# Performance work log

Measured on AMD Instinct MI355X. Metric: run time of the kernel, lower is better.

Reference implementation:

```python
import jax, jax.numpy as jnp
import numpy as np

N_NODES = 100000
F_IN = 64
F_OUT = 64
SLOPE = 0.2


def setup_inputs() -> dict:
    key = jax.random.key(0)
    k1, k2, k3, k4 = jax.random.split(key, 4)
    input_matrix = jax.random.normal(k1, (N_NODES, F_IN), dtype=jnp.float32)
    edge_index = jax.random.randint(k2, (2, 1600000), 0, N_NODES, dtype=jnp.int64)
    # xavier-uniform-style params
    lim_w = float(np.sqrt(6.0 / (F_IN + F_OUT)))
    W = jax.random.uniform(k3, (F_IN, F_OUT), minval=-lim_w, maxval=lim_w, dtype=jnp.float32)
    lim_a = float(np.sqrt(6.0 / (2 * F_OUT + 1)))
    a = jax.random.uniform(k4, (2 * F_OUT,), minval=-lim_a, maxval=lim_a, dtype=jnp.float32)
    return {"input_matrix": input_matrix, "edge_index": edge_index, "W": W, "a": a}


def reference(input_matrix, edge_index, W, a):
    N = input_matrix.shape[0]
    # add self edges
    loops = jnp.arange(N, dtype=edge_index.dtype)
    src = jnp.concatenate([edge_index[0], loops])  # [E+N]
    dst = jnp.concatenate([edge_index[1], loops])  # [E+N]

    h = input_matrix @ W                      # [N, F_out]
    F = h.shape[1]
    h_src = h[src]                            # [E+N, F_out] gather
    h_dst = h[dst]                            # [E+N, F_out] gather
    # cat([h_src, h_dst], 1) @ a == h_src @ a[:F] + h_dst @ a[F:]
    alpha = h_src @ a[:F] + h_dst @ a[F:]     # [E+N]
    alpha = jnp.where(alpha >= 0, alpha, SLOPE * alpha)  # leaky relu
    alpha = jnp.exp(alpha)
    denom = jax.ops.segment_sum(alpha, src, num_segments=N)  # [N]
    alpha = alpha / denom[src]                # segment softmax over edges sharing src
    out = jax.ops.segment_sum(h_dst * alpha[:, None], src, num_segments=N)  # [N, F_out]
    return out
```

## Files before the change

### kernel.cpp

```cpp
#include <hip/hip_runtime.h>
#include <hip/hip_bf16.h>

#define F 64
#define SLOPE 0.2f
#define NB_SHIFT 8
#define BATCH 4096
#define HIST_BLOCKS 128

typedef __attribute__((ext_vector_type(8))) short bf16x8;
typedef __attribute__((ext_vector_type(4))) float f32x4;

__device__ inline unsigned short f2bf(float f) {
    unsigned u = __float_as_uint(f);
    unsigned r = (u + 0x7FFFu + ((u >> 16) & 1u)) >> 16;
    return (unsigned short)r;
}

__global__ __launch_bounds__(256) void gat_histb(
    const int* __restrict__ src, int* __restrict__ partialHist, int E,
    const float* __restrict__ W, const float* __restrict__ a,
    unsigned short* __restrict__ Wp, float* __restrict__ w1,
    float* __restrict__ w2) {
    __shared__ int lh[512];
    int tid = threadIdx.x;
    for (int i = tid; i < 512; i += 256) lh[i] = 0;
    __syncthreads();
    for (int i = blockIdx.x * 256 + tid; i < E; i += HIST_BLOCKS * 256)
        atomicAdd(&lh[src[i] >> NB_SHIFT], 1);
    __syncthreads();
    for (int i = tid; i < 512; i += 256)
        partialHist[blockIdx.x * 512 + i] = lh[i];

    if (blockIdx.x == 0) {
        if (tid < 64) {
#pragma unroll
            for (int f = 0; f < 8; ++f) {
                int cg = f >> 1, kc = f & 1;
                int col = cg * 16 + (tid & 15);
                unsigned short us[8];
#pragma unroll
                for (int j = 0; j < 8; ++j) {
                    int k = kc * 32 + (tid >> 4) * 8 + j;
                    us[j] = f2bf(W[k * F + col]);
                }
                uint4 pk;
                pk.x = us[0] | ((unsigned)us[1] << 16);
                pk.y = us[2] | ((unsigned)us[3] << 16);
                pk.z = us[4] | ((unsigned)us[5] << 16);
                pk.w = us[6] | ((unsigned)us[7] << 16);
                *(uint4*)&Wp[(f * 64 + tid) * 8] = pk;
            }
        } else if (tid < 128) {
            int k = tid - 64;
            float acc1 = 0.f, acc2 = 0.f;
#pragma unroll
            for (int n = 0; n < F; ++n) {
                float wv = W[k * F + n];
                acc1 = fmaf(wv, a[n], acc1);
                acc2 = fmaf(wv, a[F + n], acc2);
            }
            w1[k] = acc1;
            w2[k] = acc2;
        }
    }
}

__global__ __launch_bounds__(256) void gat_gemm_mfma(
    const float* __restrict__ X, const unsigned short* __restrict__ Wp,
    const float* __restrict__ w1, const float* __restrict__ w2,
    unsigned short* __restrict__ hb, float* __restrict__ s1,
    float* __restrict__ s2, int N) {
    int tid = threadIdx.x;
    int lane = tid & 63;
    int wv = tid >> 6;
    int rowBase = blockIdx.x * 64 + wv * 16;
    if (rowBase >= N) return;
    int lrow = lane & 15;
    int kg = lane >> 4;
    int row = rowBase + lrow;
    int rclamp = (row < N) ? row : (N - 1);

    const float* xp = &X[(size_t)rclamp * F + kg * 8];
    float4 u0 = *(const float4*)(xp + 0);
    float4 u1 = *(const float4*)(xp + 4);
    float4 u2 = *(const float4*)(xp + 32);
    float4 u3 = *(const float4*)(xp + 36);
    float xr[16] = {u0.x, u0.y, u0.z, u0.w, u1.x, u1.y, u1.z, u1.w,
                    u2.x, u2.y, u2.z, u2.w, u3.x, u3.y, u3.z, u3.w};

    bf16x8 a0, a1;
#pragma unroll
    for (int j = 0; j < 8; ++j) {
        a0[j] = (short)f2bf(xr[j]);
        a1[j] = (short)f2bf(xr[8 + j]);
    }

    bf16x8 bf0 = *(const bf16x8*)&Wp[(0 * 64 + lane) * 8];
    bf16x8 bf1 = *(const bf16x8*)&Wp[(1 * 64 + lane) * 8];
    bf16x8 bf2 = *(const bf16x8*)&Wp[(2 * 64 + lane) * 8];
    bf16x8 bf3 = *(const bf16x8*)&Wp[(3 * 64 + lane) * 8];
    bf16x8 bf4 = *(const bf16x8*)&Wp[(4 * 64 + lane) * 8];
    bf16x8 bf5 = *(const bf16x8*)&Wp[(5 * 64 + lane) * 8];
    bf16x8 bf6 = *(const bf16x8*)&Wp[(6 * 64 + lane) * 8];
    bf16x8 bf7 = *(const bf16x8*)&Wp[(7 * 64 + lane) * 8];

    f32x4 acc0 = {0.f, 0.f, 0.f, 0.f};
    f32x4 acc1v = {0.f, 0.f, 0.f, 0.f};
    f32x4 acc2v = {0.f, 0.f, 0.f, 0.f};
    f32x4 acc3 = {0.f, 0.f, 0.f, 0.f};
    acc0 = __builtin_amdgcn_mfma_f32_16x16x32_bf16(a0, bf0, acc0, 0, 0, 0);
    acc0 = __builtin_amdgcn_mfma_f32_16x16x32_bf16(a1, bf1, acc0, 0, 0, 0);
    acc1v = __builtin_amdgcn_mfma_f32_16x16x32_bf16(a0, bf2, acc1v, 0, 0, 0);
    acc1v = __builtin_amdgcn_mfma_f32_16x16x32_bf16(a1, bf3, acc1v, 0, 0, 0);
    acc2v = __builtin_amdgcn_mfma_f32_16x16x32_bf16(a0, bf4, acc2v, 0, 0, 0);
    acc2v = __builtin_amdgcn_mfma_f32_16x16x32_bf16(a1, bf5, acc2v, 0, 0, 0);
    acc3 = __builtin_amdgcn_mfma_f32_16x16x32_bf16(a0, bf6, acc3, 0, 0, 0);
    acc3 = __builtin_amdgcn_mfma_f32_16x16x32_bf16(a1, bf7, acc3, 0, 0, 0);

#pragma unroll
    for (int r = 0; r < 4; ++r) {
        int ro = rowBase + kg * 4 + r;
        if (ro < N) {
            size_t rb = (size_t)ro * F + lrow;
            hb[rb + 0] = f2bf(acc0[r]);
            hb[rb + 16] = f2bf(acc1v[r]);
            hb[rb + 32] = f2bf(acc2v[r]);
            hb[rb + 48] = f2bf(acc3[r]);
        }
    }

    float4 wa0 = *(const float4*)&w1[kg * 8];
    float4 wa1 = *(const float4*)&w1[kg * 8 + 4];
    float4 wa2 = *(const float4*)&w1[32 + kg * 8];
    float4 wa3 = *(const float4*)&w1[32 + kg * 8 + 4];
    float4 wb0 = *(const float4*)&w2[kg * 8];
    float4 wb1 = *(const float4*)&w2[kg * 8 + 4];
    float4 wb2 = *(const float4*)&w2[32 + kg * 8];
    float4 wb3 = *(const float4*)&w2[32 + kg * 8 + 4];
    float wv1[16] = {wa0.x, wa0.y, wa0.z, wa0.w, wa1.x, wa1.y, wa1.z, wa1.w,
                     wa2.x, wa2.y, wa2.z, wa2.w, wa3.x, wa3.y, wa3.z, wa3.w};
    float wv2[16] = {wb0.x, wb0.y, wb0.z, wb0.w, wb1.x, wb1.y, wb1.z, wb1.w,
                     wb2.x, wb2.y, wb2.z, wb2.w, wb3.x, wb3.y, wb3.z, wb3.w};
    float p = 0.f, q = 0.f;
#pragma unroll
    for (int j = 0; j < 16; ++j) {
        p = fmaf(xr[j], wv1[j], p);
        q = fmaf(xr[j], wv2[j], q);
    }
    p += __shfl_xor(p, 16, 64);
    p += __shfl_xor(p, 32, 64);
    q += __shfl_xor(q, 16, 64);
    q += __shfl_xor(q, 32, 64);
    if (lane < 16 && row < N) {
        s1[row] = p;
        s2[row] = q;
    }
}

__global__ __launch_bounds__(512) void gat_scan0(
    const int* __restrict__ partialHist, int* __restrict__ bucketBase,
    int* __restrict__ bucketCursor, int* __restrict__ rowptrN, int NB) {
    __shared__ int wsum[8];
    int tid = threadIdx.x, lane = tid & 63, wid = tid >> 6;
    int v = 0;
    for (int p = 0; p < HIST_BLOCKS; ++p)
        v += partialHist[p * 512 + tid];
    int x = v;
#pragma unroll
    for (int off = 1; off < 64; off <<= 1) {
        int y = __shfl_up(x, off, 64);
        if (lane >= off) x += y;
    }
    if (lane == 63) wsum[wid] = x;
    __syncthreads();
    int add = 0;
    for (int w = 0; w < 8; ++w)
        if (w < wid) add += wsum[w];
    int excl = add + x - v;
    if (tid < NB) {
        bucketBase[tid] = excl;
        bucketCursor[tid] = excl;
    }
    if (tid == NB - 1) {
        bucketBase[NB] = excl + v;
        rowptrN[0] = excl + v;
    }
}

__global__ __launch_bounds__(512) void gat_bin(
    const int* __restrict__ src, const int* __restrict__ dst,
    int* __restrict__ bucketCursor, unsigned* __restrict__ bucketData, int E) {
    __shared__ int hist[512], excl[512], gbase[512], cur[512];
    __shared__ int wsum[8];
    __shared__ int2 staged[BATCH];
    int tid = threadIdx.x, lane = tid & 63, wid = tid >> 6;
    int base = blockIdx.x * BATCH;
    int n = E - base;
    if (n > BATCH) n = BATCH;

    hist[tid] = 0;
    __syncthreads();

    int se[8], de[8];
#pragma unroll
    for (int j = 0; j < 8; ++j) {
        int i = base + j * 512 + tid;
        se[j] = -1;
        de[j] = 0;
        if (i < E) {
            se[j] = src[i];
            de[j] = dst[i];
            atomicAdd(&hist[se[j] >> NB_SHIFT], 1);
        }
    }
    __syncthreads();
    int v = hist[tid];
    int x = v;
#pragma unroll
    for (int off = 1; off < 64; off <<= 1) {
        int y = __shfl_up(x, off, 64);
        if (lane >= off) x += y;
    }
    if (lane == 63) wsum[wid] = x;
    __syncthreads();
    int add = 0;
    for (int w = 0; w < 8; ++w)
        if (w < wid) add += wsum[w];
    int ex = add + x - v;
    excl[tid] = ex;
    cur[tid] = ex;
    __syncthreads();
#pragma unroll
    for (int j = 0; j < 8; ++j) {
        if (se[j] >= 0) {
            int b = se[j] >> NB_SHIFT;
            int pos = atomicAdd(&cur[b], 1);
            staged[pos] = make_int2(se[j], de[j]);
        }
    }
    if (v > 0)
        gbase[tid] = atomicAdd(&bucketCursor[tid], v);
    __syncthreads();
    for (int i = tid; i < n; i += 512) {
        int2 p = staged[i];
        int b = p.x >> NB_SHIFT;
        bucketData[gbase[b] + (i - excl[b])] =
            ((unsigned)(p.x & 255) << 24) | (unsigned)p.y;
    }
}

__global__ __launch_bounds__(256) void gat_bucket(
    const int* __restrict__ bucketBase, const unsigned* __restrict__ bucketData,
    int* __restrict__ rowptr, int* __restrict__ sortedDst, int N) {
    __shared__ int cnt[256], cur[256];
    __shared__ int wsum[4];
    int b = blockIdx.x;
    int tid = threadIdx.x, lane = tid & 63, wid = tid >> 6;
    int beg = bucketBase[b];
    int end = bucketBase[b + 1];
    int node0 = b << NB_SHIFT;

    cnt[tid] = 0;
    __syncthreads();
    for (int i = beg + tid; i < end; i += 256)
        atomicAdd(&cnt[bucketData[i] >> 24], 1);
    __syncthreads();
    int v = cnt[tid];
    int x = v;
#pragma unroll
    for (int off = 1; off < 64; off <<= 1) {
        int y = __shfl_up(x, off, 64);
        if (lane >= off) x += y;
    }
    if (lane == 63) wsum[wid] = x;
    __syncthreads();
    int add = 0;
    for (int w = 0; w < 4; ++w)
        if (w < wid) add += wsum[w];
    int excl = add + x - v;
    int node = node0 + tid;
    if (node < N) rowptr[node] = beg + excl;
    cur[tid] = beg + excl;
    __syncthreads();
    for (int i = beg + tid; i < end; i += 256) {
        unsigned w = bucketData[i];
        int pos = atomicAdd(&cur[w >> 24], 1);
        sortedDst[pos] = (int)(w & 0xFFFFFFu);
    }
}

__global__ __launch_bounds__(256) void gat_aggregate(
    const int* __restrict__ rowptr,
    const int* __restrict__ sortedDst,
    const float* __restrict__ s1, const float* __restrict__ s2,
    const unsigned short* __restrict__ hb, float* __restrict__ out, int N) {
    int tid = threadIdx.x;
    int node = blockIdx.x * 32 + (tid >> 3);
    if (node >= N) return;
    const int fo = (tid & 7) * 8;

    int beg = rowptr[node];
    int end = rowptr[node + 1];
    float s1s = s1[node];
    float as = s1s + s2[node];
    as = (as >= 0.f) ? as : SLOPE * as;
    as = expf(as);

    float accA[8], accB[8];
    {
        uint4 hv = *(const uint4*)&hb[(size_t)node * F + fo];
        accA[0] = as * __uint_as_float(hv.x << 16);
        accA[1] = as * __uint_as_float(hv.x & 0xFFFF0000u);
        accA[2] = as * __uint_as_float(hv.y << 16);
        accA[3] = as * __uint_as_float(hv.y & 0xFFFF0000u);
        accA[4] = as * __uint_as_float(hv.z << 16);
        accA[5] = as * __uint_as_float(hv.z & 0xFFFF0000u);
        accA[6] = as * __uint_as_float(hv.w << 16);
        accA[7] = as * __uint_as_float(hv.w & 0xFFFF0000u);
    }
#pragma unroll
    for (int i = 0; i < 8; ++i) accB[i] = 0.f;

    float dsum = as;
    int e = beg;
    for (; e + 2 <= end; e += 2) {
        int d0 = sortedDst[e];
        int d1 = sortedDst[e + 1];
        float t0 = s1s + s2[d0];
        float t1 = s1s + s2[d1];
        t0 = (t0 >= 0.f) ? t0 : SLOPE * t0;
        t1 = (t1 >= 0.f) ? t1 : SLOPE * t1;
        float a0 = expf(t0);
        float a1 = expf(t1);
        dsum += a0 + a1;
        uint4 g0 = *(const uint4*)&hb[(size_t)d0 * F + fo];
        uint4 g1 = *(const uint4*)&hb[(size_t)d1 * F + fo];
        accA[0] = fmaf(a0, __uint_as_float(g0.x << 16), accA[0]);
        accA[1] = fmaf(a0, __uint_as_float(g0.x & 0xFFFF0000u), accA[1]);
        accA[2] = fmaf(a0, __uint_as_float(g0.y << 16), accA[2]);
        accA[3] = fmaf(a0, __uint_as_float(g0.y & 0xFFFF0000u), accA[3]);
        accA[4] = fmaf(a0, __uint_as_float(g0.z << 16), accA[4]);
        accA[5] = fmaf(a0, __uint_as_float(g0.z & 0xFFFF0000u), accA[5]);
        accA[6] = fmaf(a0, __uint_as_float(g0.w << 16), accA[6]);
        accA[7] = fmaf(a0, __uint_as_float(g0.w & 0xFFFF0000u), accA[7]);
        accB[0] = fmaf(a1, __uint_as_float(g1.x << 16), accB[0]);
        accB[1] = fmaf(a1, __uint_as_float(g1.x & 0xFFFF0000u), accB[1]);
        accB[2] = fmaf(a1, __uint_as_float(g1.y << 16), accB[2]);
        accB[3] = fmaf(a1, __uint_as_float(g1.y & 0xFFFF0000u), accB[3]);
        accB[4] = fmaf(a1, __uint_as_float(g1.z << 16), accB[4]);
        accB[5] = fmaf(a1, __uint_as_float(g1.z & 0xFFFF0000u), accB[5]);
        accB[6] = fmaf(a1, __uint_as_float(g1.w << 16), accB[6]);
        accB[7] = fmaf(a1, __uint_as_float(g1.w & 0xFFFF0000u), accB[7]);
    }
    if (e < end) {
        int d0 = sortedDst[e];
        float t0 = s1s + s2[d0];
        t0 = (t0 >= 0.f) ? t0 : SLOPE * t0;
        float a0 = expf(t0);
        dsum += a0;
        uint4 g0 = *(const uint4*)&hb[(size_t)d0 * F + fo];
        accA[0] = fmaf(a0, __uint_as_float(g0.x << 16), accA[0]);
        accA[1] = fmaf(a0, __uint_as_float(g0.x & 0xFFFF0000u), accA[1]);
        accA[2] = fmaf(a0, __uint_as_float(g0.y << 16), accA[2]);
        accA[3] = fmaf(a0, __uint_as_float(g0.y & 0xFFFF0000u), accA[3]);
        accA[4] = fmaf(a0, __uint_as_float(g0.z << 16), accA[4]);
        accA[5] = fmaf(a0, __uint_as_float(g0.z & 0xFFFF0000u), accA[5]);
        accA[6] = fmaf(a0, __uint_as_float(g0.w << 16), accA[6]);
        accA[7] = fmaf(a0, __uint_as_float(g0.w & 0xFFFF0000u), accA[7]);
    }

    float inv = 1.0f / dsum;
    float4 r0, r1;
    r0.x = (accA[0] + accB[0]) * inv;
    r0.y = (accA[1] + accB[1]) * inv;
    r0.z = (accA[2] + accB[2]) * inv;
    r0.w = (accA[3] + accB[3]) * inv;
    r1.x = (accA[4] + accB[4]) * inv;
    r1.y = (accA[5] + accB[5]) * inv;
    r1.z = (accA[6] + accB[6]) * inv;
    r1.w = (accA[7] + accB[7]) * inv;
    *(float4*)&out[(size_t)node * F + fo] = r0;
    *(float4*)&out[(size_t)node * F + fo + 4] = r1;
}

extern "C" void kernel_launch(void* const* d_in, const int* in_sizes, int n_in,
                              void* d_out, int out_size, void* d_ws, size_t ws_size,
                              hipStream_t stream) {
    const float* X = (const float*)d_in[0];
    const int* edge = (const int*)d_in[1];
    const float* W = (const float*)d_in[2];
    const float* a = (const float*)d_in[3];

    int N = in_sizes[0] / F;
    int E = in_sizes[1] / 2;
    int NB = (N + 255) >> NB_SHIFT;

    const int* src = edge;
    const int* dst = edge + E;

    unsigned* bucketData = (unsigned*)d_ws;
    unsigned short* hb = (unsigned short*)(bucketData + E);
    float* s1 = (float*)(hb + (size_t)N * F);
    float* s2 = s1 + N;
    int* partialHist = (int*)(s2 + N);
    int* bucketBase = partialHist + HIST_BLOCKS * 512;
    int* bucketCursor = bucketBase + 513;
    int* rowptr = bucketCursor + 512;
    int* sortedDst = rowptr + (N + 1);
    unsigned short* Wp = (unsigned short*)(sortedDst + E);
    float* w1 = (float*)(Wp + 4096);
    float* w2 = w1 + 64;

    float* out = (float*)d_out;

    gat_histb<<<HIST_BLOCKS, 256, 0, stream>>>(src, partialHist, E, W, a,
                                               Wp, w1, w2);

    int gemmBlocks = (N + 63) / 64;
    gat_gemm_mfma<<<gemmBlocks, 256, 0, stream>>>(X, Wp, w1, w2, hb, s1, s2, N);

    gat_scan0<<<1, 512, 0, stream>>>(partialHist, bucketBase, bucketCursor,
                                     rowptr + N, NB);

    int binBlocks = (E + BATCH - 1) / BATCH;
    gat_bin<<<binBlocks, 512, 0, stream>>>(src, dst, bucketCursor, bucketData, E);

    gat_bucket<<<NB, 256, 0, stream>>>(bucketBase, bucketData, rowptr,
                                       sortedDst, N);

    int aggBlocks = (N + 31) / 32;
    gat_aggregate<<<aggBlocks, 256, 0, stream>>>(rowptr, sortedDst,
                                                 s1, s2, hb, out, N);
}
```

Before: 105.8 us.

## Merge histogram into GEMM launch and unroll aggregation by four edges

Weight packing moves into a small single-block prep kernel. The source histogram blocks are appended to the GEMM grid so both jobs run in one launch and share the GPU. The aggregation loop now handles four edges per iteration and issues all gathers before the exp math, which gives more memory-level parallelism. The cost is more registers in the aggregate kernel and a tiny extra serial prep launch ahead of the GEMM.

```diff
diff --git a/kernel.cpp b/kernel.cpp
--- a/kernel.cpp
+++ b/kernel.cpp
@@ -16,61 +16,65 @@
     return (unsigned short)r;
 }
 
-__global__ __launch_bounds__(256) void gat_histb(
-    const int* __restrict__ src, int* __restrict__ partialHist, int E,
+__global__ __launch_bounds__(256) void gat_prep(
     const float* __restrict__ W, const float* __restrict__ a,
     unsigned short* __restrict__ Wp, float* __restrict__ w1,
     float* __restrict__ w2) {
-    __shared__ int lh[512];
     int tid = threadIdx.x;
-    for (int i = tid; i < 512; i += 256) lh[i] = 0;
-    __syncthreads();
-    for (int i = blockIdx.x * 256 + tid; i < E; i += HIST_BLOCKS * 256)
-        atomicAdd(&lh[src[i] >> NB_SHIFT], 1);
-    __syncthreads();
-    for (int i = tid; i < 512; i += 256)
-        partialHist[blockIdx.x * 512 + i] = lh[i];
-
-    if (blockIdx.x == 0) {
-        if (tid < 64) {
-#pragma unroll
-            for (int f = 0; f < 8; ++f) {
-                int cg = f >> 1, kc = f & 1;
-                int col = cg * 16 + (tid & 15);
-                unsigned short us[8];
-#pragma unroll
-                for (int j = 0; j < 8; ++j) {
-                    int k = kc * 32 + (tid >> 4) * 8 + j;
-                    us[j] = f2bf(W[k * F + col]);
-                }
-                uint4 pk;
-                pk.x = us[0] | ((unsigned)us[1] << 16);
-                pk.y = us[2] | ((unsigned)us[3] << 16);
-                pk.z = us[4] | ((unsigned)us[5] << 16);
-                pk.w = us[6] | ((unsigned)us[7] << 16);
-                *(uint4*)&Wp[(f * 64 + tid) * 8] = pk;
+    if (tid < 64) {
+#pragma unroll
+        for (int f = 0; f < 8; ++f) {
+            int cg = f >> 1, kc = f & 1;
+            int col = cg * 16 + (tid & 15);
+            unsigned short us[8];
+#pragma unroll
+            for (int j = 0; j < 8; ++j) {
+                int k = kc * 32 + (tid >> 4) * 8 + j;
+                us[j] = f2bf(W[k * F + col]);
             }
-        } else if (tid < 128) {
-            int k = tid - 64;
-            float acc1 = 0.f, acc2 = 0.f;
-#pragma unroll
-            for (int n = 0; n < F; ++n) {
-                float wv = W[k * F + n];
-                acc1 = fmaf(wv, a[n], acc1);
-                acc2 = fmaf(wv, a[F + n], acc2);
-            }
-            w1[k] = acc1;
-            w2[k] = acc2;
+            uint4 pk;
+            pk.x = us[0] | ((unsigned)us[1] << 16);
+            pk.y = us[2] | ((unsigned)us[3] << 16);
+            pk.z = us[4] | ((unsigned)us[5] << 16);
+            pk.w = us[6] | ((unsigned)us[7] << 16);
+            *(uint4*)&Wp[(f * 64 + tid) * 8] = pk;
         }
-    }
-}
-
-__global__ __launch_bounds__(256) void gat_gemm_mfma(
+    } else if (tid < 128) {
+        int k = tid - 64;
+        float acc1 = 0.f, acc2 = 0.f;
+#pragma unroll
+        for (int n = 0; n < F; ++n) {
+            float wv = W[k * F + n];
+            acc1 = fmaf(wv, a[n], acc1);
+            acc2 = fmaf(wv, a[F + n], acc2);
+        }
+        w1[k] = acc1;
+        w2[k] = acc2;
+    }
+}
+
+__global__ __launch_bounds__(256) void gat_gemm_hist(
     const float* __restrict__ X, const unsigned short* __restrict__ Wp,
     const float* __restrict__ w1, const float* __restrict__ w2,
     unsigned short* __restrict__ hb, float* __restrict__ s1,
-    float* __restrict__ s2, int N) {
+    float* __restrict__ s2, int N,
+    const int* __restrict__ src, int* __restrict__ partialHist, int E,
+    int gemmBlocks) {
+    __shared__ int lh[512];
     int tid = threadIdx.x;
+
+    if ((int)blockIdx.x >= gemmBlocks) {
+        int hbid = blockIdx.x - gemmBlocks;
+        for (int i = tid; i < 512; i += 256) lh[i] = 0;
+        __syncthreads();
+        for (int i = hbid * 256 + tid; i < E; i += HIST_BLOCKS * 256)
+            atomicAdd(&lh[src[i] >> NB_SHIFT], 1);
+        __syncthreads();
+        for (int i = tid; i < 512; i += 256)
+            partialHist[hbid * 512 + i] = lh[i];
+        return;
+    }
+
     int lane = tid & 63;
     int wv = tid >> 6;
     int rowBase = blockIdx.x * 64 + wv * 16;
@@ -289,6 +293,16 @@
     }
 }
 
+#define EDGE_FMA(g, al, A)                                                   \
+    A[0] = fmaf(al, __uint_as_float(g.x << 16), A[0]);                       \
+    A[1] = fmaf(al, __uint_as_float(g.x & 0xFFFF0000u), A[1]);               \
+    A[2] = fmaf(al, __uint_as_float(g.y << 16), A[2]);                       \
+    A[3] = fmaf(al, __uint_as_float(g.y & 0xFFFF0000u), A[3]);               \
+    A[4] = fmaf(al, __uint_as_float(g.z << 16), A[4]);                       \
+    A[5] = fmaf(al, __uint_as_float(g.z & 0xFFFF0000u), A[5]);               \
+    A[6] = fmaf(al, __uint_as_float(g.w << 16), A[6]);                       \
+    A[7] = fmaf(al, __uint_as_float(g.w & 0xFFFF0000u), A[7]);
+
 __global__ __launch_bounds__(256) void gat_aggregate(
     const int* __restrict__ rowptr,
     const int* __restrict__ sortedDst,
@@ -323,50 +337,41 @@
 
     float dsum = as;
     int e = beg;
-    for (; e + 2 <= end; e += 2) {
+    for (; e + 4 <= end; e += 4) {
         int d0 = sortedDst[e];
         int d1 = sortedDst[e + 1];
+        int d2 = sortedDst[e + 2];
+        int d3 = sortedDst[e + 3];
         float t0 = s1s + s2[d0];
         float t1 = s1s + s2[d1];
+        float t2 = s1s + s2[d2];
+        float t3 = s1s + s2[d3];
+        uint4 g0 = *(const uint4*)&hb[(size_t)d0 * F + fo];
+        uint4 g1 = *(const uint4*)&hb[(size_t)d1 * F + fo];
+        uint4 g2 = *(const uint4*)&hb[(size_t)d2 * F + fo];
+        uint4 g3 = *(const uint4*)&hb[(size_t)d3 * F + fo];
         t0 = (t0 >= 0.f) ? t0 : SLOPE * t0;
         t1 = (t1 >= 0.f) ? t1 : SLOPE * t1;
+        t2 = (t2 >= 0.f) ? t2 : SLOPE * t2;
+        t3 = (t3 >= 0.f) ? t3 : SLOPE * t3;
         float a0 = expf(t0);
         float a1 = expf(t1);
-        dsum += a0 + a1;
-        uint4 g0 = *(const uint4*)&hb[(size_t)d0 * F + fo];
-        uint4 g1 = *(const uint4*)&hb[(size_t)d1 * F + fo];
-        accA[0] = fmaf(a0, __uint_as_float(g0.x << 16), accA[0]);
-        accA[1] = fmaf(a0, __uint_as_float(g0.x & 0xFFFF0000u), accA[1]);
-        accA[2] = fmaf(a0, __uint_as_float(g0.y << 16), accA[2]);
-        accA[3] = fmaf(a0, __uint_as_float(g0.y & 0xFFFF0000u), accA[3]);
-        accA[4] = fmaf(a0, __uint_as_float(g0.z << 16), accA[4]);
-        accA[5] = fmaf(a0, __uint_as_float(g0.z & 0xFFFF0000u), accA[5]);
-        accA[6] = fmaf(a0, __uint_as_float(g0.w << 16), accA[6]);
-        accA[7] = fmaf(a0, __uint_as_float(g0.w & 0xFFFF0000u), accA[7]);
-        accB[0] = fmaf(a1, __uint_as_float(g1.x << 16), accB[0]);
-        accB[1] = fmaf(a1, __uint_as_float(g1.x & 0xFFFF0000u), accB[1]);
-        accB[2] = fmaf(a1, __uint_as_float(g1.y << 16), accB[2]);
-        accB[3] = fmaf(a1, __uint_as_float(g1.y & 0xFFFF0000u), accB[3]);
-        accB[4] = fmaf(a1, __uint_as_float(g1.z << 16), accB[4]);
-        accB[5] = fmaf(a1, __uint_as_float(g1.z & 0xFFFF0000u), accB[5]);
-        accB[6] = fmaf(a1, __uint_as_float(g1.w << 16), accB[6]);
-        accB[7] = fmaf(a1, __uint_as_float(g1.w & 0xFFFF0000u), accB[7]);
-    }
-    if (e < end) {
+        float a2 = expf(t2);
+        float a3 = expf(t3);
+        dsum += (a0 + a1) + (a2 + a3);
+        EDGE_FMA(g0, a0, accA);
+        EDGE_FMA(g1, a1, accB);
+        EDGE_FMA(g2, a2, accA);
+        EDGE_FMA(g3, a3, accB);
+    }
+    for (; e < end; ++e) {
         int d0 = sortedDst[e];
         float t0 = s1s + s2[d0];
         t0 = (t0 >= 0.f) ? t0 : SLOPE * t0;
         float a0 = expf(t0);
         dsum += a0;
         uint4 g0 = *(const uint4*)&hb[(size_t)d0 * F + fo];
-        accA[0] = fmaf(a0, __uint_as_float(g0.x << 16), accA[0]);
-        accA[1] = fmaf(a0, __uint_as_float(g0.x & 0xFFFF0000u), accA[1]);
-        accA[2] = fmaf(a0, __uint_as_float(g0.y << 16), accA[2]);
-        accA[3] = fmaf(a0, __uint_as_float(g0.y & 0xFFFF0000u), accA[3]);
-        accA[4] = fmaf(a0, __uint_as_float(g0.z << 16), accA[4]);
-        accA[5] = fmaf(a0, __uint_as_float(g0.z & 0xFFFF0000u), accA[5]);
-        accA[6] = fmaf(a0, __uint_as_float(g0.w << 16), accA[6]);
-        accA[7] = fmaf(a0, __uint_as_float(g0.w & 0xFFFF0000u), accA[7]);
+        EDGE_FMA(g0, a0, accA);
     }
 
     float inv = 1.0f / dsum;
@@ -413,11 +418,11 @@
 
     float* out = (float*)d_out;
 
-    gat_histb<<<HIST_BLOCKS, 256, 0, stream>>>(src, partialHist, E, W, a,
-                                               Wp, w1, w2);
+    gat_prep<<<1, 256, 0, stream>>>(W, a, Wp, w1, w2);
 
     int gemmBlocks = (N + 63) / 64;
-    gat_gemm_mfma<<<gemmBlocks, 256, 0, stream>>>(X, Wp, w1, w2, hb, s1, s2, N);
+    gat_gemm_hist<<<gemmBlocks + HIST_BLOCKS, 256, 0, stream>>>(
+        X, Wp, w1, w2, hb, s1, s2, N, src, partialHist, E, gemmBlocks);
 
     gat_scan0<<<1, 512, 0, stream>>>(partialHist, bucketBase, bucketCursor,
                                      rowptr + N, NB);
```

New measurement: 105.0 us. Within noise of the previous version (-0.8%).
